# Performance work log

Hardware: AMD Instinct MI355X
Metric: run time of the kernel (lower is better)

## Reference

```python
import jax, jax.numpy as jnp
import numpy as np

NUM_TRANSFORMS = 8


def _mlp(h, W1, b1, W2, b2, W3, b3):
    h = jax.nn.relu(h @ W1 + b1)
    h = jax.nn.relu(h @ W2 + b2)
    return h @ W3 + b3


def _transforms(x, intensity):
    # x: (B,L,C), intensity: (B,K). Returns stacked (K,B,L,C).
    def t(j):
        return intensity[:, j][:, None, None]  # (B,1,1)
    outs = [
        x,                                  # 0 identity
        x * (1.0 + t(1)),                   # 1 magnitude scale up
        x + t(2),                           # 2 additive shift
        x * (1.0 - t(3)),                   # 3 magnitude scale down
        jnp.tanh(x * (1.0 + t(4))),         # 4 saturating warp
        x * jnp.exp(-t(5)),                 # 5 exponential damping
        x + t(6) * jnp.sin(x),              # 6 nonlinear perturbation
        jnp.flip(x, axis=1) + 0.0 * t(7),   # 7 time reversal
    ]
    return jnp.stack(outs, axis=0)


def setup_inputs() -> dict:
    key = jax.random.key(0)
    ks = jax.random.split(key, 16)
    B, L, C = 64, 2048, 64
    K, F, H = NUM_TRANSFORMS, 24, 64
    D = F + K  # mlp input dim = 32
    x = jax.random.normal(ks[0], (B, L, C), dtype=jnp.float32)
    prev_prob = jax.nn.softmax(jax.random.normal(ks[1], (B, K), dtype=jnp.float32), axis=-1)
    features = jax.random.normal(ks[2], (B, F), dtype=jnp.float32)
    u = jax.random.uniform(ks[3], (B, K), dtype=jnp.float32, minval=1e-6, maxval=1.0 - 1e-6)
    gumbel_noise = -jnp.log(-jnp.log(u))
    s = 0.1
    p = {
        'pW1': jax.random.normal(ks[4], (D, H)) * s, 'pb1': jnp.zeros((H,)),
        'pW2': jax.random.normal(ks[5], (H, H)) * s, 'pb2': jnp.zeros((H,)),
        'pW3': jax.random.normal(ks[6], (H, K)) * s, 'pb3': jnp.zeros((K,)),
        'iW1': jax.random.normal(ks[7], (D, H)) * s, 'ib1': jnp.zeros((H,)),
        'iW2': jax.random.normal(ks[8], (H, H)) * s, 'ib2': jnp.zeros((H,)),
        'iW3': jax.random.normal(ks[9], (H, K)) * s, 'ib3': jnp.zeros((K,)),
    }
    return dict(x=x, prev_prob=prev_prob, features=features, gumbel_noise=gumbel_noise,
                log_temperature=jnp.asarray(0.0, dtype=jnp.float32), **p)


def reference(x, prev_prob, features, gumbel_noise, log_temperature,
              pW1, pb1, pW2, pb2, pW3, pb3,
              iW1, ib1, iW2, ib2, iW3, ib3):
    K = NUM_TRANSFORMS
    mlp_in = jnp.concatenate([prev_prob, features], axis=1)  # (B, K+F)
    prob_logits = _mlp(mlp_in, pW1, pb1, pW2, pb2, pW3, pb3)           # (B,K)
    intensity = jax.nn.softplus(_mlp(mlp_in, iW1, ib1, iW2, ib2, iW3, ib3))  # (B,K)
    prob = jax.nn.softmax(prob_logits, axis=-1)
    tau = jnp.clip(jnp.exp(log_temperature), 0.01, 10.0)
    # gumbel-softmax, hard=True with straight-through estimator (training path)
    y_soft = jax.nn.softmax((prob_logits + gumbel_noise) / tau, axis=-1)
    idx = jnp.argmax(y_soft, axis=-1)
    y_hard = jax.nn.one_hot(idx, K, dtype=y_soft.dtype)
    selection = y_hard + y_soft - jax.lax.stop_gradient(y_soft)  # (B,K)
    selected_idx = jnp.argmax(selection, axis=-1)
    # compute-all-then-mask combine (dense training path _apply_mixed)
    results = _transforms(x, intensity)                 # (K,B,L,C)
    x_aug = jnp.einsum('kblc,bk->blc', results, selection)
    return x_aug, prob, intensity, selected_idx
```

## Files before the change

### kernel.cpp

```cpp
#include <hip/hip_runtime.h>

#define B_  64
#define L_  2048
#define C_  64
#define K_  8
#define F_  24
#define D_  32
#define H_  64

#define XAUG_N   (B_ * L_ * C_)
#define PROB_OFF (XAUG_N)
#define INT_OFF  (PROB_OFF + B_ * K_)
#define SEL_OFF  (INT_OFF + B_ * K_)

#define VEC_PER_BATCH   (L_ * C_ / 4)
#define BLOCKS_PER_B    16
#define VEC_PER_BLOCK   (VEC_PER_BATCH / BLOCKS_PER_B)
#define ITERS           (VEC_PER_BLOCK / 256)

__device__ __forceinline__ float softplus_f(float v) {
    return fmaxf(v, 0.f) + log1pf(expf(-fabsf(v)));
}

__global__ void __launch_bounds__(256) head_kernel(
    const float* __restrict__ prev_prob, const float* __restrict__ features,
    const float* __restrict__ gumbel,    const float* __restrict__ log_temp,
    const float* __restrict__ pW1, const float* __restrict__ pb1,
    const float* __restrict__ pW2, const float* __restrict__ pb2,
    const float* __restrict__ pW3, const float* __restrict__ pb3,
    const float* __restrict__ iW1, const float* __restrict__ ib1,
    const float* __restrict__ iW2, const float* __restrict__ ib2,
    const float* __restrict__ iW3, const float* __restrict__ ib3,
    float* __restrict__ out, float* __restrict__ ws)
{
    const int bl = threadIdx.x >> 6;
    const int h  = threadIdx.x & 63;
    const int b  = (blockIdx.x << 2) + bl;

    __shared__ float s_in[4][D_];
    __shared__ float s_a[4][H_];
    __shared__ float s_b[4][H_];
    __shared__ float s_log[4][2 * K_];

    if (h < K_)      s_in[bl][h] = prev_prob[b * K_ + h];
    else if (h < D_) s_in[bl][h] = features[b * F_ + (h - K_)];
    __syncthreads();

    float acc = pb1[h];
    #pragma unroll
    for (int d = 0; d < D_; ++d) acc = fmaf(s_in[bl][d], pW1[d * H_ + h], acc);
    s_a[bl][h] = fmaxf(acc, 0.f);
    __syncthreads();

    acc = pb2[h];
    #pragma unroll
    for (int d = 0; d < H_; ++d) acc = fmaf(s_a[bl][d], pW2[d * H_ + h], acc);
    s_b[bl][h] = fmaxf(acc, 0.f);
    __syncthreads();

    if (h < K_) {
        acc = pb3[h];
        #pragma unroll
        for (int d = 0; d < H_; ++d) acc = fmaf(s_b[bl][d], pW3[d * K_ + h], acc);
        s_log[bl][h] = acc;
    }
    __syncthreads();

    acc = ib1[h];
    #pragma unroll
    for (int d = 0; d < D_; ++d) acc = fmaf(s_in[bl][d], iW1[d * H_ + h], acc);
    s_a[bl][h] = fmaxf(acc, 0.f);
    __syncthreads();

    acc = ib2[h];
    #pragma unroll
    for (int d = 0; d < H_; ++d) acc = fmaf(s_a[bl][d], iW2[d * H_ + h], acc);
    s_b[bl][h] = fmaxf(acc, 0.f);
    __syncthreads();

    if (h < K_) {
        acc = ib3[h];
        #pragma unroll
        for (int d = 0; d < H_; ++d) acc = fmaf(s_b[bl][d], iW3[d * K_ + h], acc);
        s_log[bl][K_ + h] = acc;
    }
    __syncthreads();

    if (h == 0) {
        float plog[K_], ilog[K_];
        #pragma unroll
        for (int k = 0; k < K_; ++k) { plog[k] = s_log[bl][k]; ilog[k] = s_log[bl][K_ + k]; }

        float m = plog[0];
        #pragma unroll
        for (int k = 1; k < K_; ++k) m = fmaxf(m, plog[k]);
        float e[K_], se = 0.f;
        #pragma unroll
        for (int k = 0; k < K_; ++k) { e[k] = expf(plog[k] - m); se += e[k]; }
        #pragma unroll
        for (int k = 0; k < K_; ++k) out[PROB_OFF + b * K_ + k] = e[k] / se;

        float inten[K_];
        #pragma unroll
        for (int k = 0; k < K_; ++k) {
            inten[k] = softplus_f(ilog[k]);
            out[INT_OFF + b * K_ + k] = inten[k];
        }

        float tau = expf(log_temp[0]);
        tau = fminf(fmaxf(tau, 0.01f), 10.0f);
        float z[K_];
        float m2 = -3.4e38f;
        #pragma unroll
        for (int k = 0; k < K_; ++k) {
            z[k] = (plog[k] + gumbel[b * K_ + k]) / tau;
            m2 = fmaxf(m2, z[k]);
        }
        float se2 = 0.f;
        #pragma unroll
        for (int k = 0; k < K_; ++k) { z[k] = expf(z[k] - m2); se2 += z[k]; }
        int idx = 0; float best = z[0];
        #pragma unroll
        for (int k = 1; k < K_; ++k) { if (z[k] > best) { best = z[k]; idx = k; } }

        float ys  = best / se2;
        float sel = (1.0f + ys) - ys;
        out[SEL_OFF + b] = (float)idx;

        const float t = inten[idx];
        int kind; float p0, p1 = 0.f;
        switch (idx) {
            case 0: kind = 0; p0 = sel;                  break;
            case 1: kind = 0; p0 = sel * (1.f + t);      break;
            case 2: kind = 0; p0 = sel; p1 = sel * t;    break;
            case 3: kind = 0; p0 = sel * (1.f - t);      break;
            case 4: kind = 1; p0 = sel; p1 = 1.f + t;    break;
            case 5: kind = 0; p0 = sel * expf(-t);       break;
            case 6: kind = 2; p0 = sel; p1 = sel * t;    break;
            default: kind = 3; p0 = sel;                 break;
        }
        ws[b * 4 + 0] = (float)kind;
        ws[b * 4 + 1] = p0;
        ws[b * 4 + 2] = p1;
    }
}

__global__ void __launch_bounds__(256) apply_kernel(
    const float* __restrict__ x, const float* __restrict__ ws,
    float* __restrict__ out)
{
    const int b    = blockIdx.x >> 4;
    const int blk  = blockIdx.x & (BLOCKS_PER_B - 1);
    const int base = blk * VEC_PER_BLOCK + threadIdx.x;

    const float4* xb = (const float4*)x + (size_t)b * VEC_PER_BATCH;
    float4*       ob = (float4*)out + (size_t)b * VEC_PER_BATCH;

    const float kf = ws[b * 4 + 0];
    int kind = (int)kf;
    kind = kind < 0 ? 0 : (kind > 3 ? 3 : kind);
    const float p0 = ws[b * 4 + 1];
    const float p1 = ws[b * 4 + 2];

    float4 xv[ITERS];
    if (kind == 3) {
        #pragma unroll
        for (int i = 0; i < ITERS; ++i) {
            const int v = base + i * 256;
            const int l = v >> 4, c = v & 15;
            xv[i] = xb[(L_ - 1 - l) * 16 + c];
        }
    } else {
        #pragma unroll
        for (int i = 0; i < ITERS; ++i) xv[i] = xb[base + i * 256];
    }

    if (kind == 0) {
        #pragma unroll
        for (int i = 0; i < ITERS; ++i) {
            float4 r;
            r.x = fmaf(p0, xv[i].x, p1);
            r.y = fmaf(p0, xv[i].y, p1);
            r.z = fmaf(p0, xv[i].z, p1);
            r.w = fmaf(p0, xv[i].w, p1);
            ob[base + i * 256] = r;
        }
    } else if (kind == 1) {
        #pragma unroll
        for (int i = 0; i < ITERS; ++i) {
            float4 r;
            r.x = p0 * tanhf(p1 * xv[i].x);
            r.y = p0 * tanhf(p1 * xv[i].y);
            r.z = p0 * tanhf(p1 * xv[i].z);
            r.w = p0 * tanhf(p1 * xv[i].w);
            ob[base + i * 256] = r;
        }
    } else if (kind == 2) {
        #pragma unroll
        for (int i = 0; i < ITERS; ++i) {
            float4 r;
            r.x = fmaf(p0, xv[i].x, p1 * sinf(xv[i].x));
            r.y = fmaf(p0, xv[i].y, p1 * sinf(xv[i].y));
            r.z = fmaf(p0, xv[i].z, p1 * sinf(xv[i].z));
            r.w = fmaf(p0, xv[i].w, p1 * sinf(xv[i].w));
            ob[base + i * 256] = r;
        }
    } else {
        #pragma unroll
        for (int i = 0; i < ITERS; ++i) {
            float4 r;
            r.x = p0 * xv[i].x; r.y = p0 * xv[i].y;
            r.z = p0 * xv[i].z; r.w = p0 * xv[i].w;
            ob[base + i * 256] = r;
        }
    }
}

extern "C" void kernel_launch(void* const* d_in, const int* in_sizes, int n_in,
                              void* d_out, int out_size, void* d_ws, size_t ws_size,
                              hipStream_t stream) {
    const float* x         = (const float*)d_in[0];
    const float* prev_prob = (const float*)d_in[1];
    const float* features  = (const float*)d_in[2];
    const float* gumbel    = (const float*)d_in[3];
    const float* log_temp  = (const float*)d_in[4];
    const float* pW1 = (const float*)d_in[5];
    const float* pb1 = (const float*)d_in[6];
    const float* pW2 = (const float*)d_in[7];
    const float* pb2 = (const float*)d_in[8];
    const float* pW3 = (const float*)d_in[9];
    const float* pb3 = (const float*)d_in[10];
    const float* iW1 = (const float*)d_in[11];
    const float* ib1 = (const float*)d_in[12];
    const float* iW2 = (const float*)d_in[13];
    const float* ib2 = (const float*)d_in[14];
    const float* iW3 = (const float*)d_in[15];
    const float* ib3 = (const float*)d_in[16];

    float* out = (float*)d_out;
    float* ws  = (float*)d_ws;

    hipLaunchKernelGGL(head_kernel, dim3(B_ / 4), dim3(256), 0, stream,
                       prev_prob, features, gumbel, log_temp,
                       pW1, pb1, pW2, pb2, pW3, pb3,
                       iW1, ib1, iW2, ib2, iW3, ib3,
                       out, ws);

    hipLaunchKernelGGL(apply_kernel, dim3(B_ * BLOCKS_PER_B), dim3(256), 0, stream,
                       x, ws, out);
}
```

Measured before the change: 132.1 us.

## Fuse MLP head into apply kernel, recomputing head per block

Merges the two launches into one kernel. Each of the 1024 blocks recomputes its batch's two small MLPs and the gumbel selection, then applies the chosen transform. Only block 0 of each batch writes the prob, intensity and index outputs. This removes a kernel launch and the workspace round trip, at the cost of 16x redundant MLP work and a serial head phase at the start of every block.

```diff
diff --git a/kernel.cpp b/kernel.cpp
--- a/kernel.cpp
+++ b/kernel.cpp
@@ -22,7 +22,8 @@
     return fmaxf(v, 0.f) + log1pf(expf(-fabsf(v)));
 }
 
-__global__ void __launch_bounds__(256) head_kernel(
+__global__ void __launch_bounds__(256) fused_kernel(
+    const float* __restrict__ x,
     const float* __restrict__ prev_prob, const float* __restrict__ features,
     const float* __restrict__ gumbel,    const float* __restrict__ log_temp,
     const float* __restrict__ pW1, const float* __restrict__ pb1,
@@ -31,65 +32,76 @@
     const float* __restrict__ iW1, const float* __restrict__ ib1,
     const float* __restrict__ iW2, const float* __restrict__ ib2,
     const float* __restrict__ iW3, const float* __restrict__ ib3,
-    float* __restrict__ out, float* __restrict__ ws)
+    float* __restrict__ out)
 {
-    const int bl = threadIdx.x >> 6;
-    const int h  = threadIdx.x & 63;
-    const int b  = (blockIdx.x << 2) + bl;
-
-    __shared__ float s_in[4][D_];
-    __shared__ float s_a[4][H_];
-    __shared__ float s_b[4][H_];
-    __shared__ float s_log[4][2 * K_];
-
-    if (h < K_)      s_in[bl][h] = prev_prob[b * K_ + h];
-    else if (h < D_) s_in[bl][h] = features[b * F_ + (h - K_)];
-    __syncthreads();
-
-    float acc = pb1[h];
-    #pragma unroll
-    for (int d = 0; d < D_; ++d) acc = fmaf(s_in[bl][d], pW1[d * H_ + h], acc);
-    s_a[bl][h] = fmaxf(acc, 0.f);
-    __syncthreads();
-
-    acc = pb2[h];
-    #pragma unroll
-    for (int d = 0; d < H_; ++d) acc = fmaf(s_a[bl][d], pW2[d * H_ + h], acc);
-    s_b[bl][h] = fmaxf(acc, 0.f);
-    __syncthreads();
-
-    if (h < K_) {
-        acc = pb3[h];
-        #pragma unroll
-        for (int d = 0; d < H_; ++d) acc = fmaf(s_b[bl][d], pW3[d * K_ + h], acc);
-        s_log[bl][h] = acc;
-    }
-    __syncthreads();
-
-    acc = ib1[h];
-    #pragma unroll
-    for (int d = 0; d < D_; ++d) acc = fmaf(s_in[bl][d], iW1[d * H_ + h], acc);
-    s_a[bl][h] = fmaxf(acc, 0.f);
-    __syncthreads();
-
-    acc = ib2[h];
-    #pragma unroll
-    for (int d = 0; d < H_; ++d) acc = fmaf(s_a[bl][d], iW2[d * H_ + h], acc);
-    s_b[bl][h] = fmaxf(acc, 0.f);
-    __syncthreads();
-
-    if (h < K_) {
-        acc = ib3[h];
-        #pragma unroll
-        for (int d = 0; d < H_; ++d) acc = fmaf(s_b[bl][d], iW3[d * K_ + h], acc);
-        s_log[bl][K_ + h] = acc;
-    }
-    __syncthreads();
-
-    if (h == 0) {
+    const int b   = blockIdx.x >> 4;
+    const int blk = blockIdx.x & (BLOCKS_PER_B - 1);
+    const int tid = threadIdx.x;
+
+    __shared__ float s_in[D_];
+    __shared__ float s_a[H_];
+    __shared__ float s_b[H_];
+    __shared__ float s_log[2 * K_];
+    __shared__ float s_desc[4];
+
+    const int h = tid;
+
+    if (tid < D_) s_in[tid] = (tid < K_) ? prev_prob[b * K_ + tid]
+                                         : features[b * F_ + (tid - K_)];
+    __syncthreads();
+
+    if (tid < H_) {
+        float acc = pb1[h];
+        #pragma unroll
+        for (int d = 0; d < D_; ++d) acc = fmaf(s_in[d], pW1[d * H_ + h], acc);
+        s_a[h] = fmaxf(acc, 0.f);
+    }
+    __syncthreads();
+
+    if (tid < H_) {
+        float acc = pb2[h];
+        #pragma unroll
+        for (int d = 0; d < H_; ++d) acc = fmaf(s_a[d], pW2[d * H_ + h], acc);
+        s_b[h] = fmaxf(acc, 0.f);
+    }
+    __syncthreads();
+
+    if (tid < K_) {
+        float acc = pb3[h];
+        #pragma unroll
+        for (int d = 0; d < H_; ++d) acc = fmaf(s_b[d], pW3[d * K_ + h], acc);
+        s_log[h] = acc;
+    }
+    __syncthreads();
+
+    if (tid < H_) {
+        float acc = ib1[h];
+        #pragma unroll
+        for (int d = 0; d < D_; ++d) acc = fmaf(s_in[d], iW1[d * H_ + h], acc);
+        s_a[h] = fmaxf(acc, 0.f);
+    }
+    __syncthreads();
+
+    if (tid < H_) {
+        float acc = ib2[h];
+        #pragma unroll
+        for (int d = 0; d < H_; ++d) acc = fmaf(s_a[d], iW2[d * H_ + h], acc);
+        s_b[h] = fmaxf(acc, 0.f);
+    }
+    __syncthreads();
+
+    if (tid < K_) {
+        float acc = ib3[h];
+        #pragma unroll
+        for (int d = 0; d < H_; ++d) acc = fmaf(s_b[d], iW3[d * K_ + h], acc);
+        s_log[K_ + h] = acc;
+    }
+    __syncthreads();
+
+    if (tid == 0) {
         float plog[K_], ilog[K_];
         #pragma unroll
-        for (int k = 0; k < K_; ++k) { plog[k] = s_log[bl][k]; ilog[k] = s_log[bl][K_ + k]; }
+        for (int k = 0; k < K_; ++k) { plog[k] = s_log[k]; ilog[k] = s_log[K_ + k]; }
 
         float m = plog[0];
         #pragma unroll
@@ -97,20 +109,14 @@
         float e[K_], se = 0.f;
         #pragma unroll
         for (int k = 0; k < K_; ++k) { e[k] = expf(plog[k] - m); se += e[k]; }
-        #pragma unroll
-        for (int k = 0; k < K_; ++k) out[PROB_OFF + b * K_ + k] = e[k] / se;
 
         float inten[K_];
         #pragma unroll
-        for (int k = 0; k < K_; ++k) {
-            inten[k] = softplus_f(ilog[k]);
-            out[INT_OFF + b * K_ + k] = inten[k];
-        }
+        for (int k = 0; k < K_; ++k) inten[k] = softplus_f(ilog[k]);
 
         float tau = expf(log_temp[0]);
         tau = fminf(fmaxf(tau, 0.01f), 10.0f);
-        float z[K_];
-        float m2 = -3.4e38f;
+        float z[K_], m2 = -3.4e38f;
         #pragma unroll
         for (int k = 0; k < K_; ++k) {
             z[k] = (plog[k] + gumbel[b * K_ + k]) / tau;
@@ -125,7 +131,14 @@
 
         float ys  = best / se2;
         float sel = (1.0f + ys) - ys;
-        out[SEL_OFF + b] = (float)idx;
+
+        if (blk == 0) {
+            #pragma unroll
+            for (int k = 0; k < K_; ++k) out[PROB_OFF + b * K_ + k] = e[k] / se;
+            #pragma unroll
+            for (int k = 0; k < K_; ++k) out[INT_OFF + b * K_ + k] = inten[k];
+            out[SEL_OFF + b] = (float)idx;
+        }
 
         const float t = inten[idx];
         int kind; float p0, p1 = 0.f;
@@ -139,28 +152,18 @@
             case 6: kind = 2; p0 = sel; p1 = sel * t;    break;
             default: kind = 3; p0 = sel;                 break;
         }
-        ws[b * 4 + 0] = (float)kind;
-        ws[b * 4 + 1] = p0;
-        ws[b * 4 + 2] = p1;
-    }
-}
-
-__global__ void __launch_bounds__(256) apply_kernel(
-    const float* __restrict__ x, const float* __restrict__ ws,
-    float* __restrict__ out)
-{
-    const int b    = blockIdx.x >> 4;
-    const int blk  = blockIdx.x & (BLOCKS_PER_B - 1);
-    const int base = blk * VEC_PER_BLOCK + threadIdx.x;
-
+        s_desc[0] = (float)kind; s_desc[1] = p0; s_desc[2] = p1;
+    }
+    __syncthreads();
+
+    int kind = (int)s_desc[0];
+    kind = kind < 0 ? 0 : (kind > 3 ? 3 : kind);
+    const float p0 = s_desc[1];
+    const float p1 = s_desc[2];
+
+    const int base = blk * VEC_PER_BLOCK + tid;
     const float4* xb = (const float4*)x + (size_t)b * VEC_PER_BATCH;
     float4*       ob = (float4*)out + (size_t)b * VEC_PER_BATCH;
-
-    const float kf = ws[b * 4 + 0];
-    int kind = (int)kf;
-    kind = kind < 0 ? 0 : (kind > 3 ? 3 : kind);
-    const float p0 = ws[b * 4 + 1];
-    const float p1 = ws[b * 4 + 2];
 
     float4 xv[ITERS];
     if (kind == 3) {
@@ -238,14 +241,10 @@
     const float* ib3 = (const float*)d_in[16];
 
     float* out = (float*)d_out;
-    float* ws  = (float*)d_ws;
-
-    hipLaunchKernelGGL(head_kernel, dim3(B_ / 4), dim3(256), 0, stream,
-                       prev_prob, features, gumbel, log_temp,
+
+    hipLaunchKernelGGL(fused_kernel, dim3(B_ * BLOCKS_PER_B), dim3(256), 0, stream,
+                       x, prev_prob, features, gumbel, log_temp,
                        pW1, pb1, pW2, pb2, pW3, pb3,
                        iW1, ib1, iW2, ib2, iW3, ib3,
-                       out, ws);
-
-    hipLaunchKernelGGL(apply_kernel, dim3(B_ * BLOCKS_PER_B), dim3(256), 0, stream,
-                       x, ws, out);
+                       out);
 }
```

New measurement: 122.8 us. -7.1%, faster.
